# Kernel tuning notes

Hardware: AMD Instinct MI355X
Metric: run time of the kernel (lower is better)

## Reference

```python
import jax, jax.numpy as jnp
import numpy as np

FEAT = 1024     # args.gl_text_dim
BERT_DIM = 768
EPS = 1e-12     # torch F.normalize eps


def _conv_branch(x, W, b):
    # x: (bs, L, 768); W: (FEAT, K, 768); b: (FEAT,)
    # Equivalent to Conv2d(1, FEAT, (K, 768)) then relu, already transposed to (bs, L-K+1, FEAT)
    K = W.shape[1]
    L = x.shape[1]
    out = sum(jnp.einsum('bld,fd->blf', x[:, k:L - K + 1 + k, :], W[:, k, :]) for k in range(K))
    return jax.nn.relu(out + b)


def _l2norm(x, axis):
    n = jnp.sqrt(jnp.sum(x * x, axis=axis, keepdims=True))
    return x / jnp.maximum(n, EPS)


def setup_inputs() -> dict:
    key = jax.random.key(0)
    ks = jax.random.split(key, 10)
    bs, L = 128, 128
    def w(k, shape, fan_in):
        bound = 1.0 / np.sqrt(fan_in)
        return jax.random.uniform(k, shape, jnp.float32, -bound, bound)
    return {
        'words_emb': jax.random.normal(ks[0], (bs, L, BERT_DIM), jnp.float32),
        'sent_emb': jax.random.normal(ks[1], (bs, BERT_DIM), jnp.float32),
        'W2': w(ks[2], (FEAT, 2, BERT_DIM), 2 * BERT_DIM), 'b2': w(ks[3], (FEAT,), 2 * BERT_DIM),
        'W3': w(ks[4], (FEAT, 3, BERT_DIM), 3 * BERT_DIM), 'b3': w(ks[5], (FEAT,), 3 * BERT_DIM),
        'W4': w(ks[6], (FEAT, 4, BERT_DIM), 4 * BERT_DIM), 'b4': w(ks[7], (FEAT,), 4 * BERT_DIM),
        'Wp': w(ks[8], (FEAT, BERT_DIM), BERT_DIM), 'bp': w(ks[9], (FEAT,), BERT_DIM),
    }


def reference(words_emb, sent_emb, W2, b2, W3, b3, W4, b4, Wp, bp):
    # sentence head: dropout(eval=identity) -> linear -> l2 normalize
    sent = _l2norm(sent_emb @ Wp.T + bp, axis=-1)  # (bs, FEAT)

    L = words_emb.shape[1]  # == bert_words_num
    a = _conv_branch(words_emb, W2, b2)  # (bs, L-1, FEAT)
    b_ = _conv_branch(words_emb, W3, b3)  # (bs, L-2, FEAT)
    c = _conv_branch(words_emb, W4, b4)  # (bs, L-3, FEAT)

    seq = L - 1 - 3  # args.bert_words_num - 1 - 3
    main = jnp.maximum(jnp.maximum(a[:, :seq], b_[:, :seq]), c[:, :seq])  # (bs, seq, FEAT)
    pen = jnp.maximum(a[:, seq], b_[:, seq])[:, None]                      # (bs, 1, FEAT)
    last = a[:, seq + 1][:, None]                                          # (bs, 1, FEAT)
    code = jnp.concatenate([main, pen, last], axis=1)                      # (bs, L-2, FEAT)
    code = _l2norm(code, axis=2)
    words_out = jnp.transpose(code, (0, 2, 1))                             # (bs, FEAT, L-2)
    return words_out, sent
```

## Files before the change

kernel.cpp:

```cpp
#include <hip/hip_runtime.h>
#include <math.h>

typedef unsigned short u16;

#define BSZ 128
#define SEQL 128
#define DIM 768
#define FEAT 1024
#define WORDS_OUT_ELEMS (BSZ * FEAT * 126)

typedef __attribute__((ext_vector_type(8))) __bf16 bf16x8;
typedef __attribute__((ext_vector_type(4))) float f32x4;

__device__ __forceinline__ u16 f2bf(float x) {
  unsigned u = __float_as_uint(x);
  u += 0x7FFFu + ((u >> 16) & 1u);
  return (u16)(u >> 16);
}

__device__ __forceinline__ void gld_lds16(const void* g, void* l) {
  __builtin_amdgcn_global_load_lds(
      (const __attribute__((address_space(1))) void*)g,
      (__attribute__((address_space(3))) void*)l, 16, 0, 0);
}

#define WAITVM0 asm volatile("s_waitcnt vmcnt(0)" ::: "memory")
#define WAITVM2 asm volatile("s_waitcnt vmcnt(2)" ::: "memory")
#define WAITVM4 asm volatile("s_waitcnt vmcnt(4)" ::: "memory")

#define N4_WORDS 3145728
#define N4_W2 393216
#define N4_W3 589824
#define N4_W4 786432
#define N4_TOTAL (N4_WORDS + N4_W2 + N4_W3 + N4_W4)

__global__ __launch_bounds__(256) void cvt_all(const float* __restrict__ words,
                                               const float* __restrict__ W2,
                                               const float* __restrict__ W3,
                                               const float* __restrict__ W4,
                                               u16* __restrict__ dA, u16* __restrict__ d2,
                                               u16* __restrict__ d3, u16* __restrict__ d4) {
  int i = blockIdx.x * 256 + threadIdx.x;
  if (i >= N4_TOTAL) return;
  const float* src;
  u16* dst;
  int j = i;
  if (j < N4_WORDS) {
    src = words; dst = dA;
  } else if ((j -= N4_WORDS) < N4_W2) {
    src = W2; dst = d2;
  } else if ((j -= N4_W2) < N4_W3) {
    src = W3; dst = d3;
  } else {
    j -= N4_W3; src = W4; dst = d4;
  }
  float4 v = ((const float4*)src)[j];
  ushort4 o;
  o.x = f2bf(v.x); o.y = f2bf(v.y); o.z = f2bf(v.z); o.w = f2bf(v.w);
  ((ushort4*)dst)[j] = o;
}

__device__ __forceinline__ void stage_tile512(const u16* __restrict__ gbase, int stride,
                                              u16* __restrict__ ldsbase, int wave, int lane) {
#pragma unroll
  for (int p = 0; p < 2; ++p) {
    int slot = p * 512 + wave * 64 + lane;
    int r = slot >> 3, c = slot & 7;
    const u16* src = gbase + (size_t)r * stride + ((c ^ (r & 7)) * 8);
    unsigned uofs = __builtin_amdgcn_readfirstlane((unsigned)((p * 512 + wave * 64) * 8));
    gld_lds16(src, ldsbase + uofs);
  }
}

#define GPHASE(kc, mh, WLOAD)                                                        \
  {                                                                                  \
    bf16x8 af[4];                                                                    \
    _Pragma("unroll") for (int i = 0; i < 4; ++i) {                                  \
      int row = (mh * 4 + i) * 16 + frow + k;                                        \
      af[i] = *(const bf16x8*)&xb[(row * 8 + ((kc * 4 + fq) ^ (row & 7))) * 8];      \
    }                                                                                \
    if (WLOAD) {                                                                     \
      _Pragma("unroll") for (int ni = 0; ni < 4; ++ni) {                             \
        int row = wn + ni * 16 + frow;                                               \
        wf[ni] = *(const bf16x8*)&wcur[(row * 8 + ((kc * 4 + fq) ^ (row & 7))) * 8]; \
      }                                                                              \
    }                                                                                \
    __builtin_amdgcn_s_setprio(1);                                                   \
    _Pragma("unroll") for (int i = 0; i < 4; ++i)                                    \
        _Pragma("unroll") for (int ni = 0; ni < 4; ++ni)                             \
            acc[mh * 4 + i][ni] = __builtin_amdgcn_mfma_f32_16x16x32_bf16(           \
                af[i], wf[ni], acc[mh * 4 + i][ni], 0, 0, 0);                        \
    __builtin_amdgcn_s_setprio(0);                                                   \
    __builtin_amdgcn_sched_barrier(0);                                               \
    __builtin_amdgcn_s_barrier();                                                    \
  }

template <int K>
__device__ __forceinline__ void run_branch(const u16* __restrict__ A,
                                           const u16* __restrict__ W,
                                           const float* __restrict__ bias,
                                           u16* __restrict__ C,
                                           int b0, int tile_n, u16* lds) {
  const int KD = K * 768;
  const int Lp = 129 - K;
  const int S = 12 * K;
  const int tid = threadIdx.x;
  const int wave = tid >> 6, lane = tid & 63;
  const int frow = lane & 15;
  const int fq = lane >> 4;
  const int wq = wave >> 1;
  const int wn = (wave & 1) * 64;

  const u16* xg = A + (size_t)b0 * 98304;
  const u16* wg = W + (size_t)tile_n * 128 * KD;

  f32x4 acc[8][4];
#pragma unroll
  for (int mi = 0; mi < 8; ++mi)
#pragma unroll
    for (int ni = 0; ni < 4; ++ni) acc[mi][ni] = 0.0f;

#pragma unroll
  for (int q = 0; q < 4; ++q)
    stage_tile512(xg + (size_t)q * 98304, 768, lds + q * 8192, wave, lane);
  stage_tile512(wg, KD, lds + 65536, wave, lane);
  WAITVM0;
  __builtin_amdgcn_sched_barrier(0);
  __syncthreads();

  for (int d0i = 0; d0i < 12; ++d0i) {
    const int dd = d0i * 64;
    u16* Xcur = (d0i & 1) ? (lds + 32768) : lds;
    u16* Xnxt = (d0i & 1) ? lds : (lds + 32768);
    const u16* xb = Xcur + wq * 8192;
#pragma unroll
    for (int k = 0; k < K; ++k) {
      const int s = d0i * K + k;
      const bool lastk = (k == K - 1);
      const bool stx = lastk && (d0i < 11);
      u16* wcur = (s & 1) ? (lds + 73728) : (lds + 65536);
      u16* wnxt = (s & 1) ? (lds + 65536) : (lds + 73728);
      const int nk = lastk ? 0 : k + 1;
      const int nd = lastk ? dd + 64 : dd;

      if (s + 1 < S) stage_tile512(wg + nk * 768 + nd, KD, wnxt, wave, lane);
      if (stx) stage_tile512(xg + dd + 64, 768, Xnxt, wave, lane);
      if (s + 1 == S) { WAITVM0; } else if (stx) { WAITVM4; } else { WAITVM2; }
      __builtin_amdgcn_sched_barrier(0);
      __builtin_amdgcn_s_barrier();

      bf16x8 wf[4];
      GPHASE(0, 0, 1)
      if (stx) stage_tile512(xg + 98304 + dd + 64, 768, Xnxt + 8192, wave, lane);
      GPHASE(0, 1, 0)
      if (stx) stage_tile512(xg + 2 * 98304 + dd + 64, 768, Xnxt + 16384, wave, lane);
      GPHASE(1, 0, 1)
      if (stx) stage_tile512(xg + (size_t)3 * 98304 + dd + 64, 768, Xnxt + 24576, wave, lane);
      GPHASE(1, 1, 0)
    }
  }

  float bv[4];
#pragma unroll
  for (int ni = 0; ni < 4; ++ni) bv[ni] = bias[tile_n * 128 + wn + ni * 16 + frow];
  const int bb = b0 + wq;
#pragma unroll
  for (int mi = 0; mi < 8; ++mi) {
#pragma unroll
    for (int r = 0; r < 4; ++r) {
      int mg = mi * 16 + fq * 4 + r;
      if (mg < Lp) {
        ushort4 hs;
        hs.x = f2bf(fmaxf(acc[mi][0][r] + bv[0], 0.0f));
        hs.y = f2bf(fmaxf(acc[mi][1][r] + bv[1], 0.0f));
        hs.z = f2bf(fmaxf(acc[mi][2][r] + bv[2], 0.0f));
        hs.w = f2bf(fmaxf(acc[mi][3][r] + bv[3], 0.0f));
        *(ushort4*)(C + (size_t)(bb * Lp + mg) * FEAT + tile_n * 128 + wn + frow * 4) = hs;
      }
    }
  }
}

__global__ __launch_bounds__(512, 1) void gemm_fused(const u16* __restrict__ A,
                                                     const u16* __restrict__ W2,
                                                     const u16* __restrict__ W3,
                                                     const u16* __restrict__ W4,
                                                     const float* __restrict__ b2,
                                                     const float* __restrict__ b3,
                                                     const float* __restrict__ b4,
                                                     u16* __restrict__ Ca,
                                                     u16* __restrict__ Cb,
                                                     u16* __restrict__ Cc) {
  __shared__ u16 lds[81920];
  const int tile_n = blockIdx.x;
  const int z = blockIdx.y;
  const int b0 = blockIdx.z * 4;
  if (z == 0)
    run_branch<2>(A, W2, b2, Ca, b0, tile_n, lds);
  else if (z == 1)
    run_branch<3>(A, W3, b3, Cb, b0, tile_n, lds);
  else
    run_branch<4>(A, W4, b4, Cc, b0, tile_n, lds);
}

__device__ __forceinline__ float4 load_bf4(const u16* p) {
  uint2 q = *(const uint2*)p;
  float4 r;
  r.x = __uint_as_float((q.x & 0xFFFFu) << 16);
  r.y = __uint_as_float(q.x & 0xFFFF0000u);
  r.z = __uint_as_float((q.y & 0xFFFFu) << 16);
  r.w = __uint_as_float(q.y & 0xFFFF0000u);
  return r;
}

#define CSTR 1028

__global__ __launch_bounds__(256) void combine_norm(const u16* __restrict__ a,
                                                    const u16* __restrict__ b,
                                                    const u16* __restrict__ c,
                                                    float* __restrict__ out) {
  __shared__ float comb[16 * CSTR];
  __shared__ float red[16 * 4];
  __shared__ float inv[16];
  const int tid = threadIdx.x;
  const int wave = tid >> 6, lane = tid & 63;
  const int l0 = blockIdx.x * 16;
  const int bb = blockIdx.y;
  const int rem = (126 - l0 < 16) ? (126 - l0) : 16;
  const int f0 = tid * 4;
  const int chunk = tid >> 4, frow = tid & 15;
  const int fbase = chunk * 64 + frow;

  float part[16];
#pragma unroll
  for (int l = 0; l < 16; ++l) {
    int lg = l0 + l;
    float4 v = make_float4(0.f, 0.f, 0.f, 0.f);
    if (lg < 126) {
      v = load_bf4(a + (size_t)(bb * 127 + lg) * 1024 + f0);
      if (lg < 125) {
        float4 vb = load_bf4(b + (size_t)(bb * 126 + lg) * 1024 + f0);
        v.x = fmaxf(v.x, vb.x); v.y = fmaxf(v.y, vb.y);
        v.z = fmaxf(v.z, vb.z); v.w = fmaxf(v.w, vb.w);
      }
      if (lg < 124) {
        float4 vc = load_bf4(c + (size_t)(bb * 125 + lg) * 1024 + f0);
        v.x = fmaxf(v.x, vc.x); v.y = fmaxf(v.y, vc.y);
        v.z = fmaxf(v.z, vc.z); v.w = fmaxf(v.w, vc.w);
      }
    }
    comb[l * CSTR + fbase + 0] = v.x;
    comb[l * CSTR + fbase + 16] = v.y;
    comb[l * CSTR + fbase + 32] = v.z;
    comb[l * CSTR + fbase + 48] = v.w;
    part[l] = v.x * v.x + v.y * v.y + v.z * v.z + v.w * v.w;
  }
#pragma unroll
  for (int l = 0; l < 16; ++l) {
    float v = part[l];
    for (int off = 32; off > 0; off >>= 1) v += __shfl_down(v, off);
    if (lane == 0) red[l * 4 + wave] = v;
  }
  __syncthreads();
  if (tid < 16) {
    float s = red[tid * 4] + red[tid * 4 + 1] + red[tid * 4 + 2] + red[tid * 4 + 3];
    inv[tid] = 1.0f / fmaxf(sqrtf(s), 1e-12f);
  }
  __syncthreads();

  const int q = lane & 3, fi = lane >> 2;
  const int lb = 4 * q;
  const size_t ob = (size_t)bb * FEAT * 126;
#pragma unroll
  for (int it = 0; it < 16; ++it) {
    int f = wave * 256 + it * 16 + fi;
    if (lb + 2 <= rem) {
      float* po = out + ob + (size_t)f * 126 + l0 + lb;
      float2 w0;
      w0.x = comb[(lb + 0) * CSTR + f] * inv[lb + 0];
      w0.y = comb[(lb + 1) * CSTR + f] * inv[lb + 1];
      *(float2*)po = w0;
      if (lb + 4 <= rem) {
        float2 w1;
        w1.x = comb[(lb + 2) * CSTR + f] * inv[lb + 2];
        w1.y = comb[(lb + 3) * CSTR + f] * inv[lb + 3];
        *(float2*)(po + 2) = w1;
      }
    }
  }
}

__global__ __launch_bounds__(256) void sent_head(const float* __restrict__ se,
                                                 const float* __restrict__ Wp,
                                                 const float* __restrict__ bp,
                                                 float* __restrict__ out) {
  __shared__ float srow[768];
  __shared__ float ov[1024];
  __shared__ float red[4];
  const int b = blockIdx.x, tid = threadIdx.x;
  for (int i = tid; i < 768; i += 256) srow[i] = se[b * 768 + i];
  __syncthreads();
  float ss = 0.f;
#pragma unroll
  for (int it = 0; it < 4; ++it) {
    int f = tid + it * 256;
    const float4* w = (const float4*)(Wp + (size_t)f * 768);
    float acc = 0.f;
    for (int j = 0; j < 192; ++j) {
      float4 wv = w[j];
      float4 sv = *(const float4*)&srow[j * 4];
      acc += wv.x * sv.x + wv.y * sv.y + wv.z * sv.z + wv.w * sv.w;
    }
    acc += bp[f];
    ov[f] = acc;
    ss += acc * acc;
  }
  const int lane = tid & 63, wave = tid >> 6;
  for (int off = 32; off > 0; off >>= 1) ss += __shfl_down(ss, off);
  if (lane == 0) red[wave] = ss;
  __syncthreads();
  float tot = red[0] + red[1] + red[2] + red[3];
  float inv = 1.0f / fmaxf(sqrtf(tot), 1e-12f);
  for (int it = 0; it < 4; ++it) {
    int f = tid + it * 256;
    out[WORDS_OUT_ELEMS + (size_t)b * 1024 + f] = ov[f] * inv;
  }
}

extern "C" void kernel_launch(void* const* d_in, const int* in_sizes, int n_in,
                              void* d_out, int out_size, void* d_ws, size_t ws_size,
                              hipStream_t stream) {
  const float* words = (const float*)d_in[0];
  const float* sent = (const float*)d_in[1];
  const float* W2 = (const float*)d_in[2];
  const float* b2 = (const float*)d_in[3];
  const float* W3 = (const float*)d_in[4];
  const float* b3 = (const float*)d_in[5];
  const float* W4 = (const float*)d_in[6];
  const float* b4 = (const float*)d_in[7];
  const float* Wp = (const float*)d_in[8];
  const float* bp = (const float*)d_in[9];
  float* out = (float*)d_out;

  char* ws = (char*)d_ws;
  u16* A_bf = (u16*)(ws + 0);
  u16* W2_bf = (u16*)(ws + 25165824);
  u16* W3_bf = (u16*)(ws + 28311552);
  u16* W4_bf = (u16*)(ws + 33030144);
  u16* a_out = (u16*)(ws + 39321600);
  u16* b_out = (u16*)(ws + 72613888);
  u16* c_out = (u16*)(ws + 105644032);

  cvt_all<<<(N4_TOTAL + 255) / 256, 256, 0, stream>>>(words, W2, W3, W4,
                                                      A_bf, W2_bf, W3_bf, W4_bf);

  gemm_fused<<<dim3(8, 3, BSZ / 4), 512, 0, stream>>>(A_bf, W2_bf, W3_bf, W4_bf,
                                                      b2, b3, b4, a_out, b_out, c_out);

  combine_norm<<<dim3(8, BSZ), 256, 0, stream>>>(a_out, b_out, c_out, out);
  sent_head<<<BSZ, 256, 0, stream>>>(sent, Wp, bp, out);
}
```

Before: 503.0 us.

## Interleave weight and activation prefetch across MFMA phases with per-phase barriers

Restructures the inner GEMM pipeline: the next weight tile is split into halves issued during the first two compute phases, and the next activation chunk is prefetched at the first k-step instead of the last. Each phase now issues LDS reads plus its global-to-LDS loads, then barriers and waits on lgkmcnt before running its MFMAs, and the vmcnt wait moves to the end of the step. The goal is to spread memory traffic more evenly across compute and hide load latency. The cost is extra barriers per step and less slack before the weight buffer must land.

Measured after the change: 499.9 us. No clear change (-0.6%).

```diff
diff --git a/kernel.cpp b/kernel.cpp
--- a/kernel.cpp
+++ b/kernel.cpp
@@ -25,8 +25,7 @@
 }
 
 #define WAITVM0 asm volatile("s_waitcnt vmcnt(0)" ::: "memory")
-#define WAITVM2 asm volatile("s_waitcnt vmcnt(2)" ::: "memory")
-#define WAITVM4 asm volatile("s_waitcnt vmcnt(4)" ::: "memory")
+#define WAITVM6 asm volatile("s_waitcnt vmcnt(6)" ::: "memory")
 
 #define N4_WORDS 3145728
 #define N4_W2 393216
@@ -60,39 +59,50 @@
   ((ushort4*)dst)[j] = o;
 }
 
+__device__ __forceinline__ void stage_half(const u16* __restrict__ gbase, int stride,
+                                           u16* __restrict__ ldsbase, int half,
+                                           int wave, int lane) {
+  int slot = half * 512 + wave * 64 + lane;
+  int r = slot >> 3, c = slot & 7;
+  const u16* src = gbase + (size_t)r * stride + ((c ^ (r & 7)) * 8);
+  unsigned uofs = __builtin_amdgcn_readfirstlane((unsigned)((half * 512 + wave * 64) * 8));
+  gld_lds16(src, ldsbase + uofs);
+}
+
 __device__ __forceinline__ void stage_tile512(const u16* __restrict__ gbase, int stride,
                                               u16* __restrict__ ldsbase, int wave, int lane) {
-#pragma unroll
-  for (int p = 0; p < 2; ++p) {
-    int slot = p * 512 + wave * 64 + lane;
-    int r = slot >> 3, c = slot & 7;
-    const u16* src = gbase + (size_t)r * stride + ((c ^ (r & 7)) * 8);
-    unsigned uofs = __builtin_amdgcn_readfirstlane((unsigned)((p * 512 + wave * 64) * 8));
-    gld_lds16(src, ldsbase + uofs);
-  }
-}
-
-#define GPHASE(kc, mh, WLOAD)                                                        \
+  stage_half(gbase, stride, ldsbase, 0, wave, lane);
+  stage_half(gbase, stride, ldsbase, 1, wave, lane);
+}
+
+#define STX2(q)                                                                             \
+  {                                                                                         \
+    stage_half(xg + (size_t)(q) * 98304 + dd + 64, 768, Xnxt + (q) * 8192, 0, wave, lane);  \
+    stage_half(xg + (size_t)(q) * 98304 + dd + 64, 768, Xnxt + (q) * 8192, 1, wave, lane);  \
+  }
+
+#define PHASE(kc, mh, DUTY)                                                          \
   {                                                                                  \
-    bf16x8 af[4];                                                                    \
     _Pragma("unroll") for (int i = 0; i < 4; ++i) {                                  \
-      int row = (mh * 4 + i) * 16 + frow + k;                                        \
+      int row = mh * 64 + i * 16 + frow + k;                                         \
       af[i] = *(const bf16x8*)&xb[(row * 8 + ((kc * 4 + fq) ^ (row & 7))) * 8];      \
     }                                                                                \
-    if (WLOAD) {                                                                     \
+    if (mh == 0) {                                                                   \
       _Pragma("unroll") for (int ni = 0; ni < 4; ++ni) {                             \
         int row = wn + ni * 16 + frow;                                               \
         wf[ni] = *(const bf16x8*)&wcur[(row * 8 + ((kc * 4 + fq) ^ (row & 7))) * 8]; \
       }                                                                              \
     }                                                                                \
+    DUTY;                                                                            \
+    __builtin_amdgcn_s_barrier();                                                    \
+    asm volatile("s_waitcnt lgkmcnt(0)" ::: "memory");                               \
+    __builtin_amdgcn_sched_barrier(0);                                               \
     __builtin_amdgcn_s_setprio(1);                                                   \
     _Pragma("unroll") for (int i = 0; i < 4; ++i)                                    \
         _Pragma("unroll") for (int ni = 0; ni < 4; ++ni)                             \
             acc[mh * 4 + i][ni] = __builtin_amdgcn_mfma_f32_16x16x32_bf16(           \
                 af[i], wf[ni], acc[mh * 4 + i][ni], 0, 0, 0);                        \
     __builtin_amdgcn_s_setprio(0);                                                   \
-    __builtin_amdgcn_sched_barrier(0);                                               \
-    __builtin_amdgcn_s_barrier();                                                    \
   }
 
 template <int K>
@@ -137,26 +147,35 @@
     for (int k = 0; k < K; ++k) {
       const int s = d0i * K + k;
       const bool lastk = (k == K - 1);
-      const bool stx = lastk && (d0i < 11);
+      const bool stx = (k == 0) && (d0i < 11);
+      const bool stw = (s + 1 < S);
       u16* wcur = (s & 1) ? (lds + 73728) : (lds + 65536);
       u16* wnxt = (s & 1) ? (lds + 65536) : (lds + 73728);
       const int nk = lastk ? 0 : k + 1;
       const int nd = lastk ? dd + 64 : dd;
-
-      if (s + 1 < S) stage_tile512(wg + nk * 768 + nd, KD, wnxt, wave, lane);
-      if (stx) stage_tile512(xg + dd + 64, 768, Xnxt, wave, lane);
-      if (s + 1 == S) { WAITVM0; } else if (stx) { WAITVM4; } else { WAITVM2; }
+      const u16* wsrc = wg + nk * 768 + nd;
+
+      bf16x8 af[4], wf[4];
+      PHASE(0, 0, {
+        if (stw) stage_half(wsrc, KD, wnxt, 0, wave, lane);
+        if (stx) STX2(0);
+      })
+      __builtin_amdgcn_s_barrier();
+      PHASE(0, 1, {
+        if (stw) stage_half(wsrc, KD, wnxt, 1, wave, lane);
+        if (stx) STX2(1);
+      })
+      __builtin_amdgcn_s_barrier();
+      PHASE(1, 0, {
+        if (stx) STX2(2);
+      })
+      __builtin_amdgcn_s_barrier();
+      PHASE(1, 1, {
+        if (stx) STX2(3);
+      })
+      if (stx) { WAITVM6; } else { WAITVM0; }
       __builtin_amdgcn_sched_barrier(0);
       __builtin_amdgcn_s_barrier();
-
-      bf16x8 wf[4];
-      GPHASE(0, 0, 1)
-      if (stx) stage_tile512(xg + 98304 + dd + 64, 768, Xnxt + 8192, wave, lane);
-      GPHASE(0, 1, 0)
-      if (stx) stage_tile512(xg + 2 * 98304 + dd + 64, 768, Xnxt + 16384, wave, lane);
-      GPHASE(1, 0, 1)
-      if (stx) stage_tile512(xg + (size_t)3 * 98304 + dd + 64, 768, Xnxt + 24576, wave, lane);
-      GPHASE(1, 1, 0)
     }
   }
 
```
